# Kernel optimization log

Hardware: AMD Instinct MI355X
Metric: run time of the kernel (lower is better)

Reference implementation:

```python
import jax, jax.numpy as jnp
import numpy as np

ACT_BITS = 8  # config.activation_bits
HIDDEN = 2048
INTERMEDIATE = 4096  # hidden * mlp_ratio (2.0), power of 2
EPS = 1e-5


def fwht(x):
    """Normalized fast Walsh-Hadamard transform along last axis (n = power of 2)."""
    shape = x.shape
    n = shape[-1]
    x = x.reshape(-1, n)
    h = 1
    while h < n:  # log2(n) fixed iterations, not a data-dim loop
        x = x.reshape(-1, n // (2 * h), 2, h)
        a, b = x[:, :, 0, :], x[:, :, 1, :]
        x = jnp.stack((a + b, a - b), axis=2).reshape(-1, n)
        h *= 2
    return (x * (1.0 / np.sqrt(n))).reshape(shape)


def _ste(x, q):
    # straight-through estimator: forward uses q, backward passes grad to x
    return x + jax.lax.stop_gradient(q - x)


def act_quant(x, bits):
    """Per-token absmax quantization to `bits` bits (BitNet a8 style), dequantized."""
    qb = float(2 ** (bits - 1) - 1)
    scale = qb / jnp.clip(jnp.max(jnp.abs(x), axis=-1, keepdims=True), EPS, None)
    q = jnp.clip(jnp.round(x * scale), -qb, qb) / scale
    return _ste(x, q)


def weight_quant(w):
    """Ternary absmean weight quantization (BitNet b1.58), dequantized."""
    scale = jnp.clip(jnp.mean(jnp.abs(w)), EPS, None)
    q = jnp.clip(jnp.round(w / scale), -1.0, 1.0) * scale
    return _ste(w, q)


def hbitlinear(x, w, bits):
    # H-BitLinear: Hadamard-rotate activations, quantize acts + weights, GEMM
    xq = act_quant(fwht(x), bits)
    wq = weight_quant(w)
    return jnp.einsum('bsd,fd->bsf', xq, wq)


def setup_inputs() -> dict:
    key = jax.random.key(0)
    k1, k2, k3 = jax.random.split(key, 3)
    hidden_states = jax.random.normal(k1, (4, 4096, HIDDEN), dtype=jnp.float32)
    w_up = jax.random.normal(k2, (INTERMEDIATE, HIDDEN), dtype=jnp.float32) * 0.02
    w_down = jax.random.normal(k3, (HIDDEN, INTERMEDIATE), dtype=jnp.float32) * 0.02
    return {"hidden_states": hidden_states, "w_up": w_up, "w_down": w_down}


def reference(hidden_states, w_up, w_down):
    h = hbitlinear(hidden_states, w_up, ACT_BITS)      # (B, S, intermediate)
    h = jnp.square(jax.nn.relu(h))                     # squared ReLU
    # dropout p=0.0 -> identity in eval/reference
    return hbitlinear(h, w_down, ACT_BITS)             # (B, S, hidden)
```

## Files before the change

### kernel.cpp

```cpp
#include <hip/hip_runtime.h>
#include <hip/hip_fp16.h>
#include <cstdint>
#include <cstddef>

#define HIDDEN 2048
#define INTER  4096
#define EPSQ   1e-5f

typedef int v4i __attribute__((ext_vector_type(4)));

__device__ __forceinline__ void async_ld16(const void* g, void* l) {
  __builtin_amdgcn_global_load_lds((const __attribute__((address_space(1))) void*)g,
                                   (__attribute__((address_space(3))) void*)l, 16, 0, 0);
}

#define BAR()   __builtin_amdgcn_s_barrier()
#define LGKM0() asm volatile("s_waitcnt lgkmcnt(0)" ::: "memory")
#define VMC(n)  asm volatile("s_waitcnt vmcnt(" #n ")" ::: "memory")

__global__ void absmean_kernel(const float* __restrict__ w, size_t n4, double* __restrict__ out) {
  double s = 0.0;
  const float4* w4 = (const float4*)w;
  for (size_t i = blockIdx.x * (size_t)blockDim.x + threadIdx.x; i < n4;
       i += (size_t)gridDim.x * blockDim.x) {
    float4 v = w4[i];
    s += (double)fabsf(v.x) + (double)fabsf(v.y) + (double)fabsf(v.z) + (double)fabsf(v.w);
  }
  #pragma unroll
  for (int o = 32; o; o >>= 1) s += __shfl_down(s, o);
  __shared__ double red[4];
  if ((threadIdx.x & 63) == 0) red[threadIdx.x >> 6] = s;
  __syncthreads();
  if (threadIdx.x == 0) atomicAdd(out, red[0] + red[1] + red[2] + red[3]);
}

__global__ void quantw_kernel(const float* __restrict__ w, size_t n4,
                              const double* __restrict__ sum, double invcnt,
                              int8_t* __restrict__ q) {
  const float scale = (float)fmax(sum[0] * invcnt, (double)EPSQ);
  const float4* w4 = (const float4*)w;
  char4* q4 = (char4*)q;
  for (size_t i = blockIdx.x * (size_t)blockDim.x + threadIdx.x; i < n4;
       i += (size_t)gridDim.x * blockDim.x) {
    float4 v = w4[i];
    char4 c;
    c.x = (signed char)fmaxf(-1.f, fminf(1.f, rintf(v.x / scale)));
    c.y = (signed char)fmaxf(-1.f, fminf(1.f, rintf(v.y / scale)));
    c.z = (signed char)fmaxf(-1.f, fminf(1.f, rintf(v.z / scale)));
    c.w = (signed char)fmaxf(-1.f, fminf(1.f, rintf(v.w / scale)));
    q4[i] = c;
  }
}

template <int LOGN, bool HALF_IN>
__global__ void __launch_bounds__(256) fwht_quant_kernel(const void* __restrict__ Xv,
                                                         int8_t* __restrict__ Q,
                                                         float* __restrict__ invs) {
  constexpr int N = 1 << LOGN;
  constexpr int E = N / 64;
  const int lane = threadIdx.x & 63;
  const size_t t = (size_t)blockIdx.x * 4 + (threadIdx.x >> 6);

  float r[E];
  if constexpr (HALF_IN) {
    const int4* xp = (const int4*)((const __half*)Xv + t * (size_t)N + lane * E);
    #pragma unroll
    for (int u = 0; u < E / 8; ++u) {
      alignas(16) __half hb[8];
      *(int4*)hb = xp[u];
      #pragma unroll
      for (int j = 0; j < 8; ++j) r[u * 8 + j] = __half2float(hb[j]);
    }
  } else {
    const float4* xp = (const float4*)((const float*)Xv + t * (size_t)N + lane * E);
    #pragma unroll
    for (int u = 0; u < E / 4; ++u) {
      float4 v = xp[u];
      r[u * 4 + 0] = v.x; r[u * 4 + 1] = v.y; r[u * 4 + 2] = v.z; r[u * 4 + 3] = v.w;
    }
  }

  #pragma unroll
  for (int m = 1; m < E; m <<= 1) {
    #pragma unroll
    for (int e = 0; e < E; ++e) {
      if (!(e & m)) {
        float a = r[e], b = r[e | m];
        r[e] = a + b;
        r[e | m] = a - b;
      }
    }
  }
  #pragma unroll
  for (int m = 1; m < 64; m <<= 1) {
    const float sgn = (lane & m) ? -1.f : 1.f;
    #pragma unroll
    for (int e = 0; e < E; ++e) {
      float w = __shfl_xor(r[e], m, 64);
      r[e] = fmaf(r[e], sgn, w);
    }
  }

  float mx = 0.f;
  #pragma unroll
  for (int e = 0; e < E; ++e) mx = fmaxf(mx, fabsf(r[e]));
  #pragma unroll
  for (int m = 1; m < 64; m <<= 1) mx = fmaxf(mx, __shfl_xor(mx, m, 64));

  constexpr float c = (LOGN == 11) ? 0.022097086912079608f : 0.015625f;
  mx = fmaxf(mx * c, EPSQ);
  const float sc = 127.0f * c / mx;
  if (lane == 0) invs[t] = mx * (1.0f / 127.0f);

  alignas(16) int8_t qv[E];
  #pragma unroll
  for (int e = 0; e < E; ++e) {
    float q = rintf(r[e] * sc);
    q = fmaxf(-127.f, fminf(127.f, q));
    qv[e] = (int8_t)q;
  }
  int8_t* qp = Q + t * (size_t)N + lane * E;
  #pragma unroll
  for (int u = 0; u < E / 16; ++u) ((int4*)qp)[u] = ((const int4*)qv)[u];
}

template <bool RELU2, typename TOUT>
__global__ __launch_bounds__(512, 2)
void gemm_i8_8ph(const int8_t* __restrict__ A, const int8_t* __restrict__ B,
                 TOUT* __restrict__ C, const float* __restrict__ invs,
                 const double* __restrict__ wsum, double invcnt,
                 int N, int K) {
  __shared__ int8_t As[2 * 2 * 128 * 128];
  __shared__ int8_t Bs[2 * 2 * 128 * 128];

  const int GX = N >> 8;
  const int nwg = gridDim.x;
  int wg = blockIdx.x;
  wg = (wg & 7) * (nwg >> 3) + (wg >> 3);
  const int bx = wg % GX;
  const int by = wg / GX;
  const int m0 = by * 256, n0 = bx * 256;

  const int t = threadIdx.x;
  const int lane = t & 63;
  const int wave = t >> 6;
  const int wr = wave >> 2;
  const int wc = wave & 3;

  const int row0 = t >> 3;
  const int colsw = ((t & 7) * 16) ^ ((row0 & 7) << 4);
  const int8_t* gA0 = A + (size_t)(m0 + row0) * K + colsw;
  const int8_t* gA1 = gA0 + (size_t)128 * K;
  const int8_t* gB0 = B + (size_t)(n0 + row0) * K + colsw;
  const int8_t* gB1 = gB0 + (size_t)128 * K;
  const size_t rstep = (size_t)64 * K;

  auto SA = [&](int bf, int hf, int kt) {
    const int8_t* g = (hf ? gA1 : gA0) + (size_t)kt * 128;
    int8_t* l = As + bf * 32768 + hf * 16384 + t * 16;
    async_ld16(g, l);
    async_ld16(g + rstep, l + 8192);
  };
  auto SB = [&](int bf, int hf, int kt) {
    const int8_t* g = (hf ? gB1 : gB0) + (size_t)kt * 128;
    int8_t* l = Bs + bf * 32768 + hf * 16384 + t * 16;
    async_ld16(g, l);
    async_ld16(g + rstep, l + 8192);
  };

  const int csw0 = ((lane >> 4) * 16) ^ ((lane & 7) << 4);
  const int csw1 = (64 + (lane >> 4) * 16) ^ ((lane & 7) << 4);
  const int8_t* pA0 = As + wr * 16384 + (lane & 15) * 128;
  const int8_t* pB0 = Bs + (wc >> 1) * 16384 + ((wc & 1) * 64 + (lane & 15)) * 128;

  v4i acc[8][4] = {};
  v4i a[4][2], b[4][2];

  auto RDA = [&](int bf, int m4) {
    const int8_t* p = pA0 + bf * 32768 + m4 * 8192;
    #pragma unroll
    for (int mt = 0; mt < 4; ++mt) {
      a[mt][0] = *(const v4i*)(p + mt * 2048 + csw0);
      a[mt][1] = *(const v4i*)(p + mt * 2048 + csw1);
    }
  };
  auto RDB = [&](int bf, int n2) {
    const int8_t* p = pB0 + bf * 32768 + n2 * 4096;
    #pragma unroll
    for (int nt = 0; nt < 2; ++nt) {
      b[n2 * 2 + nt][0] = *(const v4i*)(p + nt * 2048 + csw0);
      b[n2 * 2 + nt][1] = *(const v4i*)(p + nt * 2048 + csw1);
    }
  };
  auto MM = [&](int m4, int n2) {
    __builtin_amdgcn_s_setprio(1);
    #pragma unroll
    for (int mt = 0; mt < 4; ++mt)
      #pragma unroll
      for (int nt = 0; nt < 2; ++nt) {
        v4i* c = &acc[m4 * 4 + mt][n2 * 2 + nt];
        *c = __builtin_amdgcn_mfma_i32_16x16x64_i8(a[mt][0], b[n2 * 2 + nt][0], *c, 0, 0, 0);
        *c = __builtin_amdgcn_mfma_i32_16x16x64_i8(a[mt][1], b[n2 * 2 + nt][1], *c, 0, 0, 0);
      }
    __builtin_amdgcn_s_setprio(0);
  };

  const int NIT = K >> 8;

  SA(0, 0, 0); SA(0, 1, 0); SB(0, 0, 0); SB(0, 1, 0);
  SA(1, 0, 1);
  VMC(2);
  BAR();

  for (int it = 0; it < NIT; ++it) {
    const int kt1 = 2 * it + 1, kt2 = 2 * it + 2, kt3 = 2 * it + 3;
    const bool more = it < NIT - 1;

    RDA(0, 0); RDB(0, 0);
    SA(1, 1, kt1);
    BAR(); LGKM0(); MM(0, 0); BAR();

    RDB(0, 1);
    SB(1, 0, kt1);
    BAR(); LGKM0(); MM(0, 1); BAR();

    RDA(0, 1);
    SB(1, 1, kt1);
    BAR(); LGKM0(); MM(1, 0); BAR();

    if (more) { SA(0, 0, kt2); VMC(2); } else { VMC(0); }
    BAR(); MM(1, 1); BAR();

    RDA(1, 0); RDB(1, 0);
    if (more) SA(0, 1, kt2);
    BAR(); LGKM0(); MM(0, 0); BAR();

    RDB(1, 1);
    if (more) SB(0, 0, kt2);
    BAR(); LGKM0(); MM(0, 1); BAR();

    RDA(1, 1);
    if (more) SB(0, 1, kt2);
    BAR(); LGKM0(); MM(1, 0); BAR();

    if (more) { SA(1, 0, kt3); VMC(2); }
    BAR(); MM(1, 1); BAR();
  }

  const float wscale = (float)fmax(wsum[0] * invcnt, (double)EPSQ);
  const int crow_base = m0 + wr * 128 + (lane >> 4) * 4;
  const int ccol_base = n0 + wc * 64 + (lane & 15);
  #pragma unroll
  for (int mt = 0; mt < 8; ++mt) {
    const int trow = crow_base + mt * 16;
    float fr[4];
    #pragma unroll
    for (int r = 0; r < 4; ++r) fr[r] = wscale * invs[trow + r];
    #pragma unroll
    for (int nt = 0; nt < 4; ++nt) {
      const int col = ccol_base + nt * 16;
      #pragma unroll
      for (int r = 0; r < 4; ++r) {
        float v = (float)acc[mt][nt][r] * fr[r];
        if (RELU2) v = v > 0.f ? v * v : 0.f;
        if constexpr (sizeof(TOUT) == 2)
          C[(size_t)(trow + r) * N + col] = __float2half(v);
        else
          C[(size_t)(trow + r) * N + col] = v;
      }
    }
  }
}

extern "C" void kernel_launch(void* const* d_in, const int* in_sizes, int n_in,
                              void* d_out, int out_size, void* d_ws, size_t ws_size,
                              hipStream_t stream) {
  const float* x      = (const float*)d_in[0];
  const float* w_up   = (const float*)d_in[1];
  const float* w_down = (const float*)d_in[2];
  float* out = (float*)d_out;

  const int T = in_sizes[0] / HIDDEN;
  const size_t WN = (size_t)INTER * HIDDEN;

  char* ws = (char*)d_ws;
  double* sums   = (double*)ws;
  float* invs1   = (float*)(ws + 256);
  float* invs2   = (float*)(ws + 256 + 65536);
  int8_t* wq_up  = (int8_t*)(ws + 131328);
  int8_t* wq_dn  = wq_up + WN;
  int8_t* a8_1   = wq_dn + WN;
  int8_t* a8_2   = a8_1 + (size_t)T * HIDDEN;
  __half* h      = (__half*)(a8_2 + (size_t)T * INTER);

  const double invcnt = 1.0 / (double)WN;

  hipMemsetAsync(sums, 0, 256, stream);
  absmean_kernel<<<1024, 256, 0, stream>>>(w_up, WN / 4, sums + 0);
  absmean_kernel<<<1024, 256, 0, stream>>>(w_down, WN / 4, sums + 1);
  quantw_kernel<<<2048, 256, 0, stream>>>(w_up, WN / 4, sums + 0, invcnt, wq_up);
  quantw_kernel<<<2048, 256, 0, stream>>>(w_down, WN / 4, sums + 1, invcnt, wq_dn);

  fwht_quant_kernel<11, false><<<T / 4, 256, 0, stream>>>(x, a8_1, invs1);
  gemm_i8_8ph<true, __half><<<(T / 256) * (INTER / 256), 512, 0, stream>>>(
      a8_1, wq_up, h, invs1, sums + 0, invcnt, INTER, HIDDEN);
  fwht_quant_kernel<12, true><<<T / 4, 256, 0, stream>>>(h, a8_2, invs2);
  gemm_i8_8ph<false, float><<<(T / 256) * (HIDDEN / 256), 512, 0, stream>>>(
      a8_2, wq_dn, out, invs2, sums + 1, invcnt, HIDDEN, INTER);
}
```

Baseline: 669.5 us.

## Prefetch full next k-tile up front and drop explicit LDS waits in int8 GEMM

Changes the prologue to issue both stages' A and B tiles before the loop. Inside the loop, the global-to-LDS prefetches for the next buffer are grouped so that all B and A halves are issued in two phases, followed by a vmcnt(8) wait instead of vmcnt(2). The explicit s_waitcnt lgkmcnt(0) before each MFMA group is removed and left to the compiler to insert. The aim is deeper prefetch distance and fewer forced LDS waits. The risk is wait-count correctness and stalls if the compiler's implicit waits or the new vmcnt thresholds are off.

```diff
diff --git a/kernel.cpp b/kernel.cpp
--- a/kernel.cpp
+++ b/kernel.cpp
@@ -15,7 +15,6 @@
 }
 
 #define BAR()   __builtin_amdgcn_s_barrier()
-#define LGKM0() asm volatile("s_waitcnt lgkmcnt(0)" ::: "memory")
 #define VMC(n)  asm volatile("s_waitcnt vmcnt(" #n ")" ::: "memory")
 
 __global__ void absmean_kernel(const float* __restrict__ w, size_t n4, double* __restrict__ out) {
@@ -207,43 +206,39 @@
 
   const int NIT = K >> 8;
 
-  SA(0, 0, 0); SA(0, 1, 0); SB(0, 0, 0); SB(0, 1, 0);
-  SA(1, 0, 1);
-  VMC(2);
+  SB(0, 0, 0); SB(0, 1, 0); SA(0, 0, 0); SA(0, 1, 0);
+  SB(1, 0, 1); SB(1, 1, 1); SA(1, 0, 1); SA(1, 1, 1);
+  VMC(8);
   BAR();
 
   for (int it = 0; it < NIT; ++it) {
-    const int kt1 = 2 * it + 1, kt2 = 2 * it + 2, kt3 = 2 * it + 3;
+    const int kt2 = 2 * it + 2, kt3 = 2 * it + 3;
     const bool more = it < NIT - 1;
 
     RDA(0, 0); RDB(0, 0);
-    SA(1, 1, kt1);
-    BAR(); LGKM0(); MM(0, 0); BAR();
+    BAR(); MM(0, 0); BAR();
 
     RDB(0, 1);
-    SB(1, 0, kt1);
-    BAR(); LGKM0(); MM(0, 1); BAR();
+    BAR(); MM(0, 1); BAR();
 
     RDA(0, 1);
-    SB(1, 1, kt1);
-    BAR(); LGKM0(); MM(1, 0); BAR();
-
-    if (more) { SA(0, 0, kt2); VMC(2); } else { VMC(0); }
+    if (more) { SB(0, 0, kt2); SB(0, 1, kt2); }
+    BAR(); MM(1, 0); BAR();
+
+    if (more) { SA(0, 0, kt2); SA(0, 1, kt2); VMC(8); } else { VMC(0); }
     BAR(); MM(1, 1); BAR();
 
     RDA(1, 0); RDB(1, 0);
-    if (more) SA(0, 1, kt2);
-    BAR(); LGKM0(); MM(0, 0); BAR();
+    BAR(); MM(0, 0); BAR();
 
     RDB(1, 1);
-    if (more) SB(0, 0, kt2);
-    BAR(); LGKM0(); MM(0, 1); BAR();
+    BAR(); MM(0, 1); BAR();
 
     RDA(1, 1);
-    if (more) SB(0, 1, kt2);
-    BAR(); LGKM0(); MM(1, 0); BAR();
-
-    if (more) { SA(1, 0, kt3); VMC(2); }
+    if (more) { SB(1, 0, kt3); SB(1, 1, kt3); }
+    BAR(); MM(1, 0); BAR();
+
+    if (more) { SA(1, 0, kt3); SA(1, 1, kt3); VMC(8); }
     BAR(); MM(1, 1); BAR();
   }
 
```

New measurement: 654.8 us. 1.02x faster.
